# Kernel tuning notes

Measured on AMD Instinct MI355X. Metric: run time of the kernel, lower is better.

The kernel has to match this reference:

```python
import jax, jax.numpy as jnp
import numpy as np

B, T, DIM = 2, 2048, 2048
N_HEADS, N_KV_HEADS = 16, 4
HEAD_DIM = DIM // N_HEADS  # 128
N_REP = N_HEADS // N_KV_HEADS  # 4
ROPE_THETA = 10000.0


def setup_inputs() -> dict:
    key = jax.random.key(0)
    ks = jax.random.split(key, 5)
    x = jax.random.normal(ks[0], (B, T, DIM), dtype=jnp.float32)
    # RoPE tables (equivalent to complex freqs_cis = exp(i * t * inv_freq))
    inv_freq = 1.0 / (ROPE_THETA ** (np.arange(0, HEAD_DIM, 2, dtype=np.float32) / HEAD_DIM))
    t = np.arange(T, dtype=np.float32)
    ang = np.outer(t, inv_freq)  # (T, HEAD_DIM//2)
    freqs_cos = jnp.asarray(np.cos(ang), dtype=jnp.float32)
    freqs_sin = jnp.asarray(np.sin(ang), dtype=jnp.float32)
    s = 0.02
    wq = jax.random.normal(ks[1], (DIM, N_HEADS * HEAD_DIM), dtype=jnp.float32) * s
    wk = jax.random.normal(ks[2], (DIM, N_KV_HEADS * HEAD_DIM), dtype=jnp.float32) * s
    wv = jax.random.normal(ks[3], (DIM, N_KV_HEADS * HEAD_DIM), dtype=jnp.float32) * s
    wo = jax.random.normal(ks[4], (N_HEADS * HEAD_DIM, DIM), dtype=jnp.float32) * s
    return {"x": x, "freqs_cos": freqs_cos, "freqs_sin": freqs_sin,
            "wq": wq, "wk": wk, "wv": wv, "wo": wo}


def _apply_rope(t, cos, sin):
    # t: (B, H, T, hd); cos/sin: (T, hd//2); interleaved pairs like view_as_complex
    tr = t[..., 0::2]
    ti = t[..., 1::2]
    c = cos[None, None, :, :]
    s = sin[None, None, :, :]
    out_r = tr * c - ti * s
    out_i = tr * s + ti * c
    return jnp.stack([out_r, out_i], axis=-1).reshape(t.shape)


def reference(x, freqs_cos, freqs_sin, wq, wk, wv, wo):
    Bb, Tt, C = x.shape
    q = (x @ wq).reshape(Bb, Tt, N_HEADS, HEAD_DIM).transpose(0, 2, 1, 3)      # (B,H,T,hd)
    k = (x @ wk).reshape(Bb, Tt, N_KV_HEADS, HEAD_DIM).transpose(0, 2, 1, 3)   # (B,KV,T,hd)
    v = (x @ wv).reshape(Bb, Tt, N_KV_HEADS, HEAD_DIM).transpose(0, 2, 1, 3)
    q = _apply_rope(q, freqs_cos[:Tt], freqs_sin[:Tt])
    k = _apply_rope(k, freqs_cos[:Tt], freqs_sin[:Tt])
    # GQA repeat_kv
    k = jnp.repeat(k, N_REP, axis=1)  # (B,H,T,hd)
    v = jnp.repeat(v, N_REP, axis=1)
    scale = 1.0 / jnp.sqrt(jnp.float32(HEAD_DIM))
    scores = jnp.einsum("bhqd,bhkd->bhqk", q, k) * scale
    causal = jnp.tril(jnp.ones((Tt, Tt), dtype=bool))
    scores = jnp.where(causal[None, None], scores, jnp.float32(-jnp.inf))
    attn = jax.nn.softmax(scores, axis=-1)
    out = jnp.einsum("bhqk,bhkd->bhqd", attn, v)          # (B,H,T,hd)
    out = out.transpose(0, 2, 1, 3).reshape(Bb, Tt, C)
    return out @ wo
```

## Files before the change

kernel.cpp:

```cpp
#include <hip/hip_runtime.h>
#include <hip/hip_bf16.h>

#define SEQT 2048
#define NH 16
#define HD 128

typedef __bf16 bf16;
typedef __bf16 bf16x4 __attribute__((ext_vector_type(4)));
typedef __bf16 bf16x8 __attribute__((ext_vector_type(8)));
typedef float f32x4 __attribute__((ext_vector_type(4)));

__device__ inline void glds16(const bf16* g, bf16* l) {
  __builtin_amdgcn_global_load_lds(
      (const __attribute__((address_space(1))) unsigned int*)g,
      (__attribute__((address_space(3))) unsigned int*)l, 16, 0, 0);
}

__global__ __launch_bounds__(256) void k_convert(const float* __restrict__ in,
                                                 bf16* __restrict__ out, int n8) {
  int i = blockIdx.x * 256 + threadIdx.x;
  if (i >= n8) return;
  const float4* p = (const float4*)in + (size_t)i * 2;
  float4 a = p[0], b = p[1];
  bf16x8 o;
  o[0] = (bf16)a.x; o[1] = (bf16)a.y; o[2] = (bf16)a.z; o[3] = (bf16)a.w;
  o[4] = (bf16)b.x; o[5] = (bf16)b.y; o[6] = (bf16)b.z; o[7] = (bf16)b.w;
  *((bf16x8*)out + i) = o;
}

__global__ __launch_bounds__(256) void k_transpose(const float* __restrict__ in,
                                                   bf16* __restrict__ out, int R, int C) {
  __shared__ float tile[32][33];
  int c0 = blockIdx.x * 32, r0 = blockIdx.y * 32;
  int tx = threadIdx.x, ty = threadIdx.y;
#pragma unroll
  for (int i = 0; i < 4; i++)
    tile[ty + i * 8][tx] = in[(size_t)(r0 + ty + i * 8) * C + c0 + tx];
  __syncthreads();
#pragma unroll
  for (int i = 0; i < 4; i++) {
    int r = ty + i * 8;
    out[(size_t)(c0 + r) * R + r0 + tx] = (bf16)tile[tx][r];
  }
}

template <typename OutT>
__global__ __launch_bounds__(256) void k_gemm(const bf16* __restrict__ A,
                                              const bf16* __restrict__ Bt,
                                              OutT* __restrict__ C,
                                              int M, int N, int K, int ldc) {
  __shared__ bf16 Al[128 * 32];
  __shared__ bf16 Bl[128 * 32];
  int tid = threadIdx.x;
  int m0 = blockIdx.y * 128, n0 = blockIdx.x * 128;
  int wid = tid >> 6, lane = tid & 63;
  int wr = (wid >> 1) * 64, wc = (wid & 1) * 64;
  int lr = lane & 15, lk = (lane >> 4) * 8;
  f32x4 acc[4][4] = {};

  for (int k0 = 0; k0 < K; k0 += 32) {
#pragma unroll
    for (int i = 0; i < 2; i++) {
      int idx = i * 256 + tid;
      int r = idx >> 2, kc = (idx & 3) * 8;
      glds16(A + (size_t)(m0 + r) * K + k0 + kc, Al + idx * 8);
      glds16(Bt + (size_t)(n0 + r) * K + k0 + kc, Bl + idx * 8);
    }
    __syncthreads();
    bf16x8 af[4], bfr[4];
#pragma unroll
    for (int mi = 0; mi < 4; mi++) af[mi] = *(const bf16x8*)&Al[(wr + mi * 16 + lr) * 32 + lk];
#pragma unroll
    for (int ni = 0; ni < 4; ni++) bfr[ni] = *(const bf16x8*)&Bl[(wc + ni * 16 + lr) * 32 + lk];
#pragma unroll
    for (int mi = 0; mi < 4; mi++)
#pragma unroll
      for (int ni = 0; ni < 4; ni++)
        acc[mi][ni] = __builtin_amdgcn_mfma_f32_16x16x32_bf16(af[mi], bfr[ni], acc[mi][ni], 0, 0, 0);
    __syncthreads();
  }

  int rbase = m0 + wr + ((lane >> 4) << 2);
#pragma unroll
  for (int mi = 0; mi < 4; mi++)
#pragma unroll
    for (int ni = 0; ni < 4; ni++)
#pragma unroll
      for (int r = 0; r < 4; r++) {
        int row = rbase + mi * 16 + r;
        int col = n0 + wc + ni * 16 + lr;
        C[(size_t)row * ldc + col] = (OutT)acc[mi][ni][r];
      }
}

__global__ __launch_bounds__(256) void k_rope(bf16* __restrict__ qkv,
                                              const float* __restrict__ fcos,
                                              const float* __restrict__ fsin) {
  int gid = blockIdx.x * 256 + threadIdx.x;
  int row = gid / 1280;
  int p = gid % 1280;
  int head = p >> 6;
  int dp = p & 63;
  int t = row & (SEQT - 1);
  int colbase = head < NH ? head * HD : NH * HD + (head - NH) * HD;
  bf16* ptr = qkv + (size_t)row * 3072 + colbase + dp * 2;
  float a = (float)ptr[0], b = (float)ptr[1];
  float c = fcos[t * 64 + dp], s = fsin[t * 64 + dp];
  ptr[0] = (bf16)(a * c - b * s);
  ptr[1] = (bf16)(a * s + b * c);
}

__global__ __launch_bounds__(256, 3) void k_attn(const bf16* __restrict__ qkv,
                                                 bf16* __restrict__ attout) {
  __shared__ bf16 Kl[64 * 128];
  __shared__ bf16 Vt[128][72];
  __shared__ bf16 Pl[4][16][72];
  int bid = blockIdx.x;
  int qt = 31 - (bid >> 5);
  int bh = bid & 31;
  int b = bh >> 4, h = bh & 15, kvh = h >> 2;
  int tid = threadIdx.x, wid = tid >> 6, lane = tid & 63;
  int lr = lane & 15;
  int g = lane >> 4;
  int g4 = g * 4, g8 = g * 8, g16 = g * 16;
  int swz = (lr & 7) << 4;
  int q0 = qt * 64;
  const float scale = 0.08838834764831845f;

  const bf16* kgbase = qkv + (size_t)b * SEQT * 3072 + 2048 + kvh * HD;
  const bf16* vgbase = kgbase + 512;

  bf16x8 qf[4];
  {
    const bf16* qb = qkv + (size_t)(b * SEQT + q0 + wid * 16 + lr) * 3072 + h * HD;
#pragma unroll
    for (int db = 0; db < 4; db++) qf[db] = *(const bf16x8*)(qb + db * 32 + g8);
  }
  float mrun[4] = {-INFINITY, -INFINITY, -INFINITY, -INFINITY};
  float lrun[4] = {0.f, 0.f, 0.f, 0.f};
  f32x4 o[8] = {};
  int nkt = qt + 1;
  int qg0 = q0 + wid * 16 + g4;

  int kq4 = (wid * 4 + g) * 4;
  int dc = lr * 8;
  int xr = (lr & 7) << 3;
  int kvw = kq4 ^ xr;

  for (int kt = 0; kt < nkt; kt++) {
    int kv0 = kt * 64;
#pragma unroll
    for (int r = 0; r < 4; r++) {
      int ci = r * 256 + tid;
      int row = ci >> 4;
      int sl = (ci & 15) ^ (row & 7);
      glds16(kgbase + (size_t)(kv0 + row) * 3072 + sl * 8, Kl + ci * 8);
    }
    {
      const bf16* vrow = vgbase + (size_t)(kv0 + kq4) * 3072 + dc;
      bf16x8 vv0 = *(const bf16x8*)(vrow);
      bf16x8 vv1 = *(const bf16x8*)(vrow + 3072);
      bf16x8 vv2 = *(const bf16x8*)(vrow + 6144);
      bf16x8 vv3 = *(const bf16x8*)(vrow + 9216);
#pragma unroll
      for (int j = 0; j < 8; j++) {
        bf16x4 w;
        w[0] = vv0[j]; w[1] = vv1[j]; w[2] = vv2[j]; w[3] = vv3[j];
        *(bf16x4*)&Vt[dc + j][kvw] = w;
      }
    }
    __syncthreads();

    f32x4 s[4] = {};
    __builtin_amdgcn_s_setprio(1);
#pragma unroll
    for (int cb = 0; cb < 4; cb++) {
      const char* krow = (const char*)(Kl + (cb * 16 + lr) * 128);
#pragma unroll
      for (int db = 0; db < 4; db++) {
        bf16x8 kf = *(const bf16x8*)(krow + ((db * 64 + g16) ^ swz));
        s[cb] = __builtin_amdgcn_mfma_f32_16x16x32_bf16(qf[db], kf, s[cb], 0, 0, 0);
      }
    }
    __builtin_amdgcn_s_setprio(0);

    float pv[4][4];
    float rmax[4] = {-INFINITY, -INFINITY, -INFINITY, -INFINITY};
#pragma unroll
    for (int cb = 0; cb < 4; cb++) {
      int kvg = kv0 + cb * 16 + lr;
#pragma unroll
      for (int r = 0; r < 4; r++) {
        float v = s[cb][r] * scale;
        if (kvg > qg0 + r) v = -INFINITY;
        pv[cb][r] = v;
        rmax[r] = fmaxf(rmax[r], v);
      }
    }
#pragma unroll
    for (int mk = 1; mk <= 8; mk <<= 1)
#pragma unroll
      for (int r = 0; r < 4; r++) rmax[r] = fmaxf(rmax[r], __shfl_xor(rmax[r], mk));
    float alpha[4], rsum[4] = {0.f, 0.f, 0.f, 0.f};
#pragma unroll
    for (int r = 0; r < 4; r++) {
      float mnew = fmaxf(mrun[r], rmax[r]);
      alpha[r] = __expf(mrun[r] - mnew);
      mrun[r] = mnew;
    }
#pragma unroll
    for (int cb = 0; cb < 4; cb++)
#pragma unroll
      for (int r = 0; r < 4; r++) {
        float e = __expf(pv[cb][r] - mrun[r]);
        pv[cb][r] = e;
        rsum[r] += e;
      }
#pragma unroll
    for (int mk = 1; mk <= 8; mk <<= 1)
#pragma unroll
      for (int r = 0; r < 4; r++) rsum[r] += __shfl_xor(rsum[r], mk);
#pragma unroll
    for (int r = 0; r < 4; r++) lrun[r] = lrun[r] * alpha[r] + rsum[r];
#pragma unroll
    for (int df = 0; df < 8; df++)
#pragma unroll
      for (int r = 0; r < 4; r++) o[df][r] *= alpha[r];

#pragma unroll
    for (int cb = 0; cb < 4; cb++)
#pragma unroll
      for (int r = 0; r < 4; r++)
        Pl[wid][g4 + r][cb * 16 + lr] = (bf16)pv[cb][r];

    __builtin_amdgcn_s_setprio(1);
#pragma unroll
    for (int kb = 0; kb < 2; kb++) {
      bf16x8 pa = *(const bf16x8*)&Pl[wid][lr][kb * 32 + g8];
#pragma unroll
      for (int df = 0; df < 8; df++) {
        int d = df * 16 + lr;
        int xv = ((d >> 3) & 7) << 3;
        bf16x8 vb = *(const bf16x8*)&Vt[d][(kb * 32 + g8) ^ xv];
        o[df] = __builtin_amdgcn_mfma_f32_16x16x32_bf16(pa, vb, o[df], 0, 0, 0);
      }
    }
    __builtin_amdgcn_s_setprio(0);
    __syncthreads();
  }

#pragma unroll
  for (int r = 0; r < 4; r++) {
    float inv = 1.f / lrun[r];
    int qg = q0 + wid * 16 + g4 + r;
    bf16* ob = attout + (size_t)(b * SEQT + qg) * 2048 + h * HD;
#pragma unroll
    for (int df = 0; df < 8; df++)
      ob[df * 16 + lr] = (bf16)(o[df][r] * inv);
  }
}

extern "C" void kernel_launch(void* const* d_in, const int* in_sizes, int n_in,
                              void* d_out, int out_size, void* d_ws, size_t ws_size,
                              hipStream_t stream) {
  const float* x    = (const float*)d_in[0];
  const float* fcos = (const float*)d_in[1];
  const float* fsin = (const float*)d_in[2];
  const float* wq   = (const float*)d_in[3];
  const float* wk   = (const float*)d_in[4];
  const float* wv   = (const float*)d_in[5];
  const float* wo   = (const float*)d_in[6];
  float* out = (float*)d_out;

  char* ws = (char*)d_ws;
  bf16* XB  = (bf16*)ws;
  bf16* W   = (bf16*)(ws + 16777216);
  bf16* QKV = (bf16*)(ws + 16777216 + 12582912);

  dim3 tb(32, 8);
  k_transpose<<<dim3(64, 64), tb, 0, stream>>>(wq, W, 2048, 2048);
  k_transpose<<<dim3(16, 64), tb, 0, stream>>>(wk, W + 2048 * 2048, 2048, 512);
  k_transpose<<<dim3(16, 64), tb, 0, stream>>>(wv, W + 2560 * 2048, 2048, 512);
  k_convert<<<4096, 256, 0, stream>>>(x, XB, 1048576);
  k_gemm<bf16><<<dim3(24, 32), 256, 0, stream>>>(XB, W, QKV, 4096, 3072, 2048, 3072);
  k_rope<<<20480, 256, 0, stream>>>(QKV, fcos, fsin);
  k_attn<<<1024, 256, 0, stream>>>(QKV, XB);
  k_transpose<<<dim3(64, 64), tb, 0, stream>>>(wo, W, 2048, 2048);
  k_gemm<float><<<dim3(16, 32), 256, 0, stream>>>(XB, W, out, 4096, 2048, 2048, 2048);
}
```

Before: 256.3 us.

## Double-buffer K tiles, prefetch V into registers, and skip most softmax rescales

The attention kernel now double-buffers the K tile in LDS and keeps the next V tile in registers, issuing the next tile's global loads before the current tile's compute. This hides global-load latency behind the MFMA work. It also defers the per-tile row-sum shuffles to one reduction at the end. The running max and output rescale are updated only when some row's max grows by more than 8, otherwise a stale max is used. Occupancy hint drops from 3 to 2 blocks per CU to make room for the extra LDS and registers. This could lower latency hiding through occupancy, and the lazy rescale leans on fp32 headroom.

```diff
diff --git a/kernel.cpp b/kernel.cpp
--- a/kernel.cpp
+++ b/kernel.cpp
@@ -110,9 +110,9 @@
   ptr[1] = (bf16)(a * s + b * c);
 }
 
-__global__ __launch_bounds__(256, 3) void k_attn(const bf16* __restrict__ qkv,
+__global__ __launch_bounds__(256, 2) void k_attn(const bf16* __restrict__ qkv,
                                                  bf16* __restrict__ attout) {
-  __shared__ bf16 Kl[64 * 128];
+  __shared__ bf16 Kl[2][64 * 128];
   __shared__ bf16 Vt[128][72];
   __shared__ bf16 Pl[4][16][72];
   int bid = blockIdx.x;
@@ -137,7 +137,7 @@
     for (int db = 0; db < 4; db++) qf[db] = *(const bf16x8*)(qb + db * 32 + g8);
   }
   float mrun[4] = {-INFINITY, -INFINITY, -INFINITY, -INFINITY};
-  float lrun[4] = {0.f, 0.f, 0.f, 0.f};
+  float lpart[4] = {0.f, 0.f, 0.f, 0.f};
   f32x4 o[8] = {};
   int nkt = qt + 1;
   int qg0 = q0 + wid * 16 + g4;
@@ -147,35 +147,62 @@
   int xr = (lr & 7) << 3;
   int kvw = kq4 ^ xr;
 
+  bf16x8 vr0, vr1, vr2, vr3;
+
+#pragma unroll
+  for (int r = 0; r < 4; r++) {
+    int ci = r * 256 + tid;
+    int row = ci >> 4;
+    int sl = (ci & 15) ^ (row & 7);
+    glds16(kgbase + (size_t)row * 3072 + sl * 8, &Kl[0][ci * 8]);
+  }
+  {
+    const bf16* vrow = vgbase + (size_t)kq4 * 3072 + dc;
+    vr0 = *(const bf16x8*)(vrow);
+    vr1 = *(const bf16x8*)(vrow + 3072);
+    vr2 = *(const bf16x8*)(vrow + 6144);
+    vr3 = *(const bf16x8*)(vrow + 9216);
+  }
+
   for (int kt = 0; kt < nkt; kt++) {
+    int cur = kt & 1;
+    asm volatile("s_waitcnt vmcnt(0)" ::: "memory");
+
+#pragma unroll
+    for (int j = 0; j < 8; j++) {
+      bf16x4 w;
+      w[0] = vr0[j]; w[1] = vr1[j]; w[2] = vr2[j]; w[3] = vr3[j];
+      *(bf16x4*)&Vt[dc + j][kvw] = w;
+    }
+
+    if (kt + 1 < nkt) {
+      int kv1 = (kt + 1) * 64;
+      bf16* kdst = &Kl[(kt + 1) & 1][0];
+#pragma unroll
+      for (int r = 0; r < 4; r++) {
+        int ci = r * 256 + tid;
+        int row = ci >> 4;
+        int sl = (ci & 15) ^ (row & 7);
+        glds16(kgbase + (size_t)(kv1 + row) * 3072 + sl * 8, kdst + ci * 8);
+      }
+      const bf16* vrow = vgbase + (size_t)(kv1 + kq4) * 3072 + dc;
+      vr0 = *(const bf16x8*)(vrow);
+      vr1 = *(const bf16x8*)(vrow + 3072);
+      vr2 = *(const bf16x8*)(vrow + 6144);
+      vr3 = *(const bf16x8*)(vrow + 9216);
+    }
+
+    asm volatile("s_waitcnt lgkmcnt(0)" ::: "memory");
+    __builtin_amdgcn_sched_barrier(0);
+    __builtin_amdgcn_s_barrier();
+    __builtin_amdgcn_sched_barrier(0);
+
     int kv0 = kt * 64;
-#pragma unroll
-    for (int r = 0; r < 4; r++) {
-      int ci = r * 256 + tid;
-      int row = ci >> 4;
-      int sl = (ci & 15) ^ (row & 7);
-      glds16(kgbase + (size_t)(kv0 + row) * 3072 + sl * 8, Kl + ci * 8);
-    }
-    {
-      const bf16* vrow = vgbase + (size_t)(kv0 + kq4) * 3072 + dc;
-      bf16x8 vv0 = *(const bf16x8*)(vrow);
-      bf16x8 vv1 = *(const bf16x8*)(vrow + 3072);
-      bf16x8 vv2 = *(const bf16x8*)(vrow + 6144);
-      bf16x8 vv3 = *(const bf16x8*)(vrow + 9216);
-#pragma unroll
-      for (int j = 0; j < 8; j++) {
-        bf16x4 w;
-        w[0] = vv0[j]; w[1] = vv1[j]; w[2] = vv2[j]; w[3] = vv3[j];
-        *(bf16x4*)&Vt[dc + j][kvw] = w;
-      }
-    }
-    __syncthreads();
-
     f32x4 s[4] = {};
     __builtin_amdgcn_s_setprio(1);
 #pragma unroll
     for (int cb = 0; cb < 4; cb++) {
-      const char* krow = (const char*)(Kl + (cb * 16 + lr) * 128);
+      const char* krow = (const char*)(&Kl[cur][0] + (cb * 16 + lr) * 128);
 #pragma unroll
       for (int db = 0; db < 4; db++) {
         bf16x8 kf = *(const bf16x8*)(krow + ((db * 64 + g16) ^ swz));
@@ -185,7 +212,7 @@
     __builtin_amdgcn_s_setprio(0);
 
     float pv[4][4];
-    float rmax[4] = {-INFINITY, -INFINITY, -INFINITY, -INFINITY};
+    float pmax[4] = {-INFINITY, -INFINITY, -INFINITY, -INFINITY};
 #pragma unroll
     for (int cb = 0; cb < 4; cb++) {
       int kvg = kv0 + cb * 16 + lr;
@@ -194,38 +221,37 @@
         float v = s[cb][r] * scale;
         if (kvg > qg0 + r) v = -INFINITY;
         pv[cb][r] = v;
-        rmax[r] = fmaxf(rmax[r], v);
+        pmax[r] = fmaxf(pmax[r], v);
       }
     }
 #pragma unroll
     for (int mk = 1; mk <= 8; mk <<= 1)
 #pragma unroll
-      for (int r = 0; r < 4; r++) rmax[r] = fmaxf(rmax[r], __shfl_xor(rmax[r], mk));
-    float alpha[4], rsum[4] = {0.f, 0.f, 0.f, 0.f};
+      for (int r = 0; r < 4; r++) pmax[r] = fmaxf(pmax[r], __shfl_xor(pmax[r], mk));
+    float grow = fmaxf(fmaxf(pmax[0] - mrun[0], pmax[1] - mrun[1]),
+                       fmaxf(pmax[2] - mrun[2], pmax[3] - mrun[3]));
+    if (!__all(grow <= 8.0f)) {
+#pragma unroll
+      for (int r = 0; r < 4; r++) {
+        float mnew = fmaxf(mrun[r], pmax[r]);
+        float alpha = __expf(mrun[r] - mnew);
+        mrun[r] = mnew;
+        lpart[r] *= alpha;
+#pragma unroll
+        for (int df = 0; df < 8; df++) o[df][r] *= alpha;
+      }
+    }
 #pragma unroll
     for (int r = 0; r < 4; r++) {
-      float mnew = fmaxf(mrun[r], rmax[r]);
-      alpha[r] = __expf(mrun[r] - mnew);
-      mrun[r] = mnew;
-    }
-#pragma unroll
-    for (int cb = 0; cb < 4; cb++)
-#pragma unroll
-      for (int r = 0; r < 4; r++) {
+      float rs = 0.f;
+#pragma unroll
+      for (int cb = 0; cb < 4; cb++) {
         float e = __expf(pv[cb][r] - mrun[r]);
         pv[cb][r] = e;
-        rsum[r] += e;
-      }
-#pragma unroll
-    for (int mk = 1; mk <= 8; mk <<= 1)
-#pragma unroll
-      for (int r = 0; r < 4; r++) rsum[r] += __shfl_xor(rsum[r], mk);
-#pragma unroll
-    for (int r = 0; r < 4; r++) lrun[r] = lrun[r] * alpha[r] + rsum[r];
-#pragma unroll
-    for (int df = 0; df < 8; df++)
-#pragma unroll
-      for (int r = 0; r < 4; r++) o[df][r] *= alpha[r];
+        rs += e;
+      }
+      lpart[r] += rs;
+    }
 
 #pragma unroll
     for (int cb = 0; cb < 4; cb++)
@@ -246,12 +272,18 @@
       }
     }
     __builtin_amdgcn_s_setprio(0);
-    __syncthreads();
-  }
-
+    __builtin_amdgcn_sched_barrier(0);
+    __builtin_amdgcn_s_barrier();
+    __builtin_amdgcn_sched_barrier(0);
+  }
+
+#pragma unroll
+  for (int mk = 1; mk <= 8; mk <<= 1)
+#pragma unroll
+    for (int r = 0; r < 4; r++) lpart[r] += __shfl_xor(lpart[r], mk);
 #pragma unroll
   for (int r = 0; r < 4; r++) {
-    float inv = 1.f / lrun[r];
+    float inv = 1.f / lpart[r];
     int qg = q0 + wid * 16 + g4 + r;
     bf16* ob = attout + (size_t)(b * SEQT + qg) * 2048 + h * HD;
 #pragma unroll
```

Result: faster. 242.2 us (-5.5%).
